# Kernel optimization log

Hardware: AMD Instinct MI355X
Metric: run time of the kernel (lower is better)

The kernel has to match this reference:

```python
import jax, jax.numpy as jnp
import numpy as np

EMBED_DIM = 1024
NUM_HEADS = 16
HEAD_DIM = EMBED_DIM // NUM_HEADS
SCALING = HEAD_DIM ** (-0.5)
LN_EPS = 1e-5


def setup_inputs() -> dict:
    key = jax.random.key(0)
    ks = jax.random.split(key, 6)
    N, L, D = 2, 2048, EMBED_DIM
    x = jax.random.normal(ks[0], (N, L, D), dtype=jnp.float32)
    W_in = jax.random.normal(ks[1], (3 * D, D), dtype=jnp.float32) * 0.02
    b_in = jnp.zeros((3 * D,), dtype=jnp.float32)
    Wc = jax.random.normal(ks[2], (HEAD_DIM, HEAD_DIM), dtype=jnp.float32) * 0.1
    bc = jnp.zeros((HEAD_DIM,), dtype=jnp.float32)
    ln_gamma = jnp.ones((HEAD_DIM,), dtype=jnp.float32)
    ln_beta = jnp.zeros((HEAD_DIM,), dtype=jnp.float32)
    W_out = jax.random.normal(ks[3], (D, D), dtype=jnp.float32) * 0.02
    b_out = jnp.zeros((D,), dtype=jnp.float32)
    return {"x": x, "W_in": W_in, "b_in": b_in, "Wc": Wc, "bc": bc,
            "ln_gamma": ln_gamma, "ln_beta": ln_beta, "W_out": W_out, "b_out": b_out}


def _reshape_heads(t, N, L):
    # (N, L, D) -> (N*H, L, head_dim)
    return t.reshape(N, L, NUM_HEADS, HEAD_DIM).transpose(0, 2, 1, 3).reshape(N * NUM_HEADS, L, HEAD_DIM)


def reference(x, W_in, b_in, Wc, bc, ln_gamma, ln_beta, W_out, b_out):
    N, L, D = x.shape
    qkv = jnp.einsum('nld,ed->nle', x, W_in) + b_in  # (N, L, 3D)
    q, k, v = jnp.split(qkv, 3, axis=-1)
    q_head = _reshape_heads(q, N, L)  # (B, L, HD) with B = N*H
    k_head = _reshape_heads(k, N, L)
    v_head = _reshape_heads(v, N, L)

    # Conv1d with kernel_size=1 == pointwise linear on head_dim channels
    q_temp = jnp.einsum('blc,oc->blo', q_head, Wc) + bc
    q_temp = jax.nn.gelu(q_temp, approximate=False)  # torch nn.GELU() is exact erf
    mu = q_temp.mean(axis=-1, keepdims=True)
    var = q_temp.var(axis=-1, keepdims=True)
    q_temp = (q_temp - mu) / jnp.sqrt(var + LN_EPS) * ln_gamma + ln_beta

    q_rel = q_temp.mean(axis=1)  # (B, HD) -- mean over sequence
    # one kernel row per (batch, head): (B, L)
    W_kernel_row = jnp.einsum('bd,bld->bl', q_rel * SCALING, k_head)

    # Toeplitz attention matrix: attn[b, i, j] = W_kernel_row[b, |i-j|]
    idx = jnp.arange(L)
    lags = jnp.abs(idx[:, None] - idx[None, :])  # (L, L), already in [0, L-1]
    attn = W_kernel_row[:, lags]  # (B, L, L) gather

    causal_mask = lags * jnp.sign(idx[None, :] - idx[:, None]) > 0  # j > i
    causal_mask = jnp.triu(jnp.ones((L, L), dtype=bool), k=1)
    attn = jnp.where(causal_mask[None, :, :], -jnp.inf, attn)
    weights = jax.nn.softmax(attn, axis=-1)  # (B, L, L); dropout=0 -> identity

    attn_out = jnp.einsum('bij,bjd->bid', weights, v_head)  # (B, L, HD)
    attn_out = attn_out.reshape(N, NUM_HEADS, L, HEAD_DIM).transpose(0, 2, 1, 3).reshape(N, L, D)
    output = jnp.einsum('nld,ed->nle', attn_out, W_out) + b_out
    return output, weights.mean(axis=1)
```

## Files before the change

kernel.cpp:

```cpp
#include <hip/hip_runtime.h>
#include <math.h>

#define L_SEQ 2048
#define D_EMB 1024
#define NHEADS 16
#define HD 64
#define BHEADS 32
#define NBATCH 2
#define LN_EPS 1e-5f
#define SCALING 0.125f

typedef __attribute__((ext_vector_type(8))) __bf16 bf16x8;
typedef __attribute__((ext_vector_type(4))) float f32x4;
typedef const __attribute__((address_space(1))) unsigned int* gptr_as1;
typedef __attribute__((address_space(3))) unsigned int* lptr_as3;

__device__ __forceinline__ void load16_to_lds(const void* g, void* l) {
  __builtin_amdgcn_global_load_lds((gptr_as1)g, (lptr_as3)l, 16, 0, 0);
}

__device__ __forceinline__ unsigned short f2bf(float f) {
  unsigned int u = __float_as_uint(f);
  u += 0x7fff + ((u >> 16) & 1);
  return (unsigned short)(u >> 16);
}

__global__ __launch_bounds__(256) void cvt4_bf16_kernel(
    const float* __restrict__ a, int na, const float* __restrict__ b, int nb,
    const float* __restrict__ c, int nc, const float* __restrict__ d, int nd,
    unsigned short* __restrict__ oa, unsigned short* __restrict__ ob,
    unsigned short* __restrict__ oc, unsigned short* __restrict__ od) {
  int i = (blockIdx.x * 256 + threadIdx.x) * 4;
  const float* src;
  unsigned short* dst;
  int j;
  if (i < na) { src = a; dst = oa; j = i; }
  else if (i < na + nb) { src = b; dst = ob; j = i - na; }
  else if (i < na + nb + nc) { src = c; dst = oc; j = i - na - nb; }
  else if (i < na + nb + nc + nd) { src = d; dst = od; j = i - na - nb - nc; }
  else return;
  float4 v = *(const float4*)&src[j];
  ushort4 o;
  o.x = f2bf(v.x); o.y = f2bf(v.y); o.z = f2bf(v.z); o.w = f2bf(v.w);
  *(ushort4*)&dst[j] = o;
}

__global__ __launch_bounds__(256) void gemm_qkv(
    const unsigned short* __restrict__ A, const unsigned short* __restrict__ B,
    const float* __restrict__ bias, unsigned short* __restrict__ Cbf,
    unsigned short* __restrict__ vT, int M, int Nn, int K) {
  __shared__ unsigned short As[4096];
  __shared__ unsigned short Bs[4096];
  const int id = blockIdx.y * 24 + blockIdx.x;
  const int by = (id / 48) * 2 + (id & 1);
  const int bx = (id % 48) >> 1;
  const int bm = by * 128;
  const int bn = bx * 128;
  const int tid = threadIdx.x;
  const int lane = tid & 63;
  const int wave = tid >> 6;
  const int wr = (wave >> 1) * 64;
  const int wc = (wave & 1) * 64;

  const int c0 = tid, c1 = tid + 256;
  const unsigned short* ga0 = A + (size_t)(bm + (c0 >> 6) * 16 + (c0 & 15)) * K + ((c0 >> 4) & 3) * 8;
  const unsigned short* ga1 = A + (size_t)(bm + (c1 >> 6) * 16 + (c1 & 15)) * K + ((c1 >> 4) & 3) * 8;
  const unsigned short* gb0 = B + (size_t)(bn + (c0 >> 6) * 16 + (c0 & 15)) * K + ((c0 >> 4) & 3) * 8;
  const unsigned short* gb1 = B + (size_t)(bn + (c1 >> 6) * 16 + (c1 & 15)) * K + ((c1 >> 4) & 3) * 8;

  f32x4 acc[4][4] = {};
  for (int k0 = 0; k0 < K; k0 += 32) {
    load16_to_lds(ga0 + k0, &As[c0 * 8]);
    load16_to_lds(ga1 + k0, &As[c1 * 8]);
    load16_to_lds(gb0 + k0, &Bs[c0 * 8]);
    load16_to_lds(gb1 + k0, &Bs[c1 * 8]);
    __syncthreads();
    bf16x8 af[4], bf[4];
    #pragma unroll
    for (int i = 0; i < 4; ++i)
      af[i] = *(const bf16x8*)&As[((wr >> 4) + i) * 512 + lane * 8];
    #pragma unroll
    for (int j = 0; j < 4; ++j)
      bf[j] = *(const bf16x8*)&Bs[((wc >> 4) + j) * 512 + lane * 8];
    #pragma unroll
    for (int i = 0; i < 4; ++i)
      #pragma unroll
      for (int j = 0; j < 4; ++j)
        acc[i][j] = __builtin_amdgcn_mfma_f32_16x16x32_bf16(af[i], bf[j], acc[i][j], 0, 0, 0);
    __syncthreads();
  }
  const int lc = lane & 15;
  const int lr4 = (lane >> 4) << 2;
  float bv[4];
  #pragma unroll
  for (int j = 0; j < 4; ++j) bv[j] = bias[bn + wc + j * 16 + lc];
  if (bn < 2 * D_EMB) {
    #pragma unroll
    for (int i = 0; i < 4; ++i)
      #pragma unroll
      for (int r = 0; r < 4; ++r) {
        const int row = bm + wr + i * 16 + lr4 + r;
        unsigned short* cp = &Cbf[(size_t)row * Nn + bn + wc + lc];
        #pragma unroll
        for (int j = 0; j < 4; ++j) cp[j * 16] = f2bf(acc[i][j][r] + bv[j]);
      }
  } else {
    #pragma unroll
    for (int i = 0; i < 4; ++i) {
      const int row0 = bm + wr + i * 16 + lr4;
      const int n = row0 >> 11;
      const int jseq = row0 & (L_SEQ - 1);
      #pragma unroll
      for (int j = 0; j < 4; ++j) {
        const int col = bn + wc + j * 16 + lc;
        const int d = col & 63;
        const int h = (col >> 6) & 15;
        ushort4 o;
        o.x = f2bf(acc[i][j][0] + bv[j]);
        o.y = f2bf(acc[i][j][1] + bv[j]);
        o.z = f2bf(acc[i][j][2] + bv[j]);
        o.w = f2bf(acc[i][j][3] + bv[j]);
        *(ushort4*)&vT[(size_t)((n * 16 + h) * 64 + d) * L_SEQ + jseq] = o;
      }
    }
  }
}

__global__ __launch_bounds__(256) void gemm_out64(
    const unsigned short* __restrict__ A, const unsigned short* __restrict__ B,
    const float* __restrict__ bias, float* __restrict__ C,
    int M, int Nn, int K) {
  __shared__ unsigned short As[2048];
  __shared__ unsigned short Bs[4096];
  const int bm = blockIdx.y * 64;
  const int bn = blockIdx.x * 128;
  const int tid = threadIdx.x;
  const int lane = tid & 63;
  const int wave = tid >> 6;
  const int wr = (wave >> 1) * 32;
  const int wc = (wave & 1) * 64;

  const int ca = tid;
  const int cb0 = tid, cb1 = tid + 256;
  const unsigned short* ga = A + (size_t)(bm + (ca >> 6) * 16 + (ca & 15)) * K + ((ca >> 4) & 3) * 8;
  const unsigned short* gb0 = B + (size_t)(bn + (cb0 >> 6) * 16 + (cb0 & 15)) * K + ((cb0 >> 4) & 3) * 8;
  const unsigned short* gb1 = B + (size_t)(bn + (cb1 >> 6) * 16 + (cb1 & 15)) * K + ((cb1 >> 4) & 3) * 8;

  f32x4 acc[2][4] = {};
  for (int k0 = 0; k0 < K; k0 += 32) {
    load16_to_lds(ga + k0, &As[ca * 8]);
    load16_to_lds(gb0 + k0, &Bs[cb0 * 8]);
    load16_to_lds(gb1 + k0, &Bs[cb1 * 8]);
    __syncthreads();
    bf16x8 af[2], bf[4];
    #pragma unroll
    for (int i = 0; i < 2; ++i)
      af[i] = *(const bf16x8*)&As[((wr >> 4) + i) * 512 + lane * 8];
    #pragma unroll
    for (int j = 0; j < 4; ++j)
      bf[j] = *(const bf16x8*)&Bs[((wc >> 4) + j) * 512 + lane * 8];
    #pragma unroll
    for (int i = 0; i < 2; ++i)
      #pragma unroll
      for (int j = 0; j < 4; ++j)
        acc[i][j] = __builtin_amdgcn_mfma_f32_16x16x32_bf16(af[i], bf[j], acc[i][j], 0, 0, 0);
    __syncthreads();
  }
  const int lc = lane & 15;
  const int lr4 = (lane >> 4) << 2;
  float bv[4];
  #pragma unroll
  for (int j = 0; j < 4; ++j) bv[j] = bias[bn + wc + j * 16 + lc];
  #pragma unroll
  for (int i = 0; i < 2; ++i)
    #pragma unroll
    for (int r = 0; r < 4; ++r) {
      const int row = bm + wr + i * 16 + lr4 + r;
      float* cp = &C[(size_t)row * Nn + bn + wc + lc];
      #pragma unroll
      for (int j = 0; j < 4; ++j) cp[j * 16] = acc[i][j][r] + bv[j];
    }
}

__global__ __launch_bounds__(256) void qtemp_mfma_kernel(
    const unsigned short* __restrict__ qkv_bf, const unsigned short* __restrict__ Wc_bf,
    const float* __restrict__ bc, const float* __restrict__ gamma,
    const float* __restrict__ beta, float* __restrict__ q_rel_sum) {
  __shared__ unsigned short Qs[8192];
  __shared__ unsigned short Ws[4096];
  __shared__ float red[4][64];
  const int b = blockIdx.y;
  const int n = b >> 4, h = b & 15;
  const int l0 = blockIdx.x * 128;
  const int tid = threadIdx.x;
  const int lane = tid & 63;
  const int wave = tid >> 6;
  const int quad = lane >> 4;
  const int mi = lane & 15;

  #pragma unroll
  for (int s = 0; s < 4; ++s) {
    const int c = tid + s * 256;
    const int row = ((c >> 7) << 4) + (c & 15);
    const int kof = ((c >> 4) & 7) << 3;
    load16_to_lds(qkv_bf + (size_t)(n * L_SEQ + l0 + row) * (3 * D_EMB) + h * 64 + kof,
                  &Qs[c * 8]);
  }
  #pragma unroll
  for (int s = 0; s < 2; ++s) {
    const int c = tid + s * 256;
    const int row = ((c >> 7) << 4) + (c & 15);
    const int kof = ((c >> 4) & 7) << 3;
    load16_to_lds(Wc_bf + row * 64 + kof, &Ws[c * 8]);
  }
  __syncthreads();

  f32x4 acc[2][4] = {};
  #pragma unroll
  for (int kk = 0; kk < 2; ++kk) {
    const int fo = ((kk * 4 + quad) * 16 + mi) * 8;
    bf16x8 bf[4];
    #pragma unroll
    for (int t = 0; t < 4; ++t) bf[t] = *(const bf16x8*)&Ws[t * 1024 + fo];
    #pragma unroll
    for (int isub = 0; isub < 2; ++isub) {
      const bf16x8 af = *(const bf16x8*)&Qs[(wave * 2 + isub) * 1024 + fo];
      #pragma unroll
      for (int t = 0; t < 4; ++t)
        acc[isub][t] = __builtin_amdgcn_mfma_f32_16x16x32_bf16(af, bf[t], acc[isub][t], 0, 0, 0);
    }
  }

  float bcv[4], gav[4], bev[4], colacc[4];
  #pragma unroll
  for (int t = 0; t < 4; ++t) {
    const int col = t * 16 + mi;
    bcv[t] = bc[col]; gav[t] = gamma[col]; bev[t] = beta[col];
    colacc[t] = 0.f;
  }
  #pragma unroll
  for (int isub = 0; isub < 2; ++isub) {
    #pragma unroll
    for (int r = 0; r < 4; ++r) {
      float g[4];
      float s1 = 0.f, s2 = 0.f;
      #pragma unroll
      for (int t = 0; t < 4; ++t) {
        const float d = acc[isub][t][r] + bcv[t];
        const float gg = 0.5f * d * (1.f + erff(d * 0.70710678118654752f));
        g[t] = gg;
        s1 += gg;
        s2 += gg * gg;
      }
      #pragma unroll
      for (int off = 8; off > 0; off >>= 1) {
        s1 += __shfl_xor(s1, off);
        s2 += __shfl_xor(s2, off);
      }
      const float mu = s1 * (1.f / 64.f);
      const float var = s2 * (1.f / 64.f) - mu * mu;
      const float rs = rsqrtf(var + LN_EPS);
      #pragma unroll
      for (int t = 0; t < 4; ++t)
        colacc[t] += (g[t] - mu) * rs * gav[t] + bev[t];
    }
  }
  #pragma unroll
  for (int t = 0; t < 4; ++t) {
    colacc[t] += __shfl_xor(colacc[t], 16);
    colacc[t] += __shfl_xor(colacc[t], 32);
  }
  if (quad == 0) {
    #pragma unroll
    for (int t = 0; t < 4; ++t) red[wave][t * 16 + mi] = colacc[t];
  }
  __syncthreads();
  if (wave == 0) {
    float tot = red[0][lane] + red[1][lane] + red[2][lane] + red[3][lane];
    atomicAdd(&q_rel_sum[b * 64 + lane], tot);
  }
}

__global__ __launch_bounds__(256) void wrow_kernel(
    const unsigned short* __restrict__ qkv_bf, const float* __restrict__ q_rel_sum,
    float* __restrict__ w_row) {
  const int b = blockIdx.x;
  const int n = b >> 4, h = b & 15;
  __shared__ float q_s[64];
  const int tid = threadIdx.x;
  if (tid < 64) q_s[tid] = q_rel_sum[b * 64 + tid] * (SCALING / (float)L_SEQ);
  __syncthreads();
  const int t = blockIdx.y * 256 + tid;
  const unsigned short* kp = &qkv_bf[(size_t)(n * L_SEQ + t) * (3 * D_EMB) + D_EMB + h * 64];
  float acc = 0.f;
  #pragma unroll
  for (int c = 0; c < 64; c += 8) {
    uint4 kv = *(const uint4*)&kp[c];
    acc += q_s[c + 0] * __uint_as_float(kv.x << 16);
    acc += q_s[c + 1] * __uint_as_float(kv.x & 0xffff0000u);
    acc += q_s[c + 2] * __uint_as_float(kv.y << 16);
    acc += q_s[c + 3] * __uint_as_float(kv.y & 0xffff0000u);
    acc += q_s[c + 4] * __uint_as_float(kv.z << 16);
    acc += q_s[c + 5] * __uint_as_float(kv.z & 0xffff0000u);
    acc += q_s[c + 6] * __uint_as_float(kv.w << 16);
    acc += q_s[c + 7] * __uint_as_float(kv.w & 0xffff0000u);
  }
  w_row[b * L_SEQ + t] = acc;
}

__global__ __launch_bounds__(256) void scan_kernel(
    const float* __restrict__ w_row, float* __restrict__ e_out,
    float* __restrict__ inv_out) {
  const int b = blockIdx.x;
  const int tid = threadIdx.x;
  __shared__ float sh[L_SEQ];
  __shared__ float ts[256];
  const float* wb = w_row + b * L_SEQ;
  float m = -3.4e38f;
  for (int i = tid; i < L_SEQ; i += 256) {
    float v = wb[i];
    sh[i] = v;
    m = fmaxf(m, v);
  }
  ts[tid] = m;
  __syncthreads();
  for (int off = 128; off > 0; off >>= 1) {
    if (tid < off) ts[tid] = fmaxf(ts[tid], ts[tid + off]);
    __syncthreads();
  }
  const float mx = ts[0];
  __syncthreads();
  const int t0 = tid * 8;
  float loc[8];
  float run = 0.f;
  #pragma unroll
  for (int k = 0; k < 8; ++k) {
    float ev = expf(sh[t0 + k] - mx);
    e_out[b * L_SEQ + t0 + k] = ev;
    run += ev;
    loc[k] = run;
  }
  ts[tid] = run;
  __syncthreads();
  for (int off = 1; off < 256; off <<= 1) {
    float v = ts[tid];
    float add = (tid >= off) ? ts[tid - off] : 0.f;
    __syncthreads();
    ts[tid] = v + add;
    __syncthreads();
  }
  float prefix = (tid > 0) ? ts[tid - 1] : 0.f;
  #pragma unroll
  for (int k = 0; k < 8; ++k)
    inv_out[b * L_SEQ + t0 + k] = 1.f / (prefix + loc[k]);
}

__global__ __launch_bounds__(256) void conv_mfma_kernel(
    const unsigned short* __restrict__ vT, const float* __restrict__ e_arr,
    const float* __restrict__ inv_arr, unsigned short* __restrict__ attn_out) {
  __shared__ unsigned short V_s[2][2048];
  __shared__ unsigned short rep[2][8 * 320];
  const int blk = 7 - blockIdx.x;
  const int b = blockIdx.y;
  const int dh = blockIdx.z;
  const int n = b >> 4, h = b & 15;
  const int blkI = blk * 256;
  const int blk4 = blk * 4;
  const int njt = blk4 + 4;
  const int tid = threadIdx.x;
  const int lane = tid & 63;
  const int wave = tid >> 6;
  const int quad = lane >> 4;
  const int mi = lane & 15;
  const float* e_b = e_arr + b * L_SEQ;

  const unsigned short* vsrc = vT +
      (size_t)(b * 64 + dh * 32 + (tid >> 7) * 16 + (tid & 15)) * L_SEQ + ((tid >> 4) & 7) * 8;

  f32x4 acc[4][2] = {};

  {
    load16_to_lds(vsrc, &V_s[0][tid * 8]);
    const int lagBase = blkI;
    int v = tid;
    int lag = lagBase + 256 - v;
    float ev = (lag >= 0 && lag < L_SEQ) ? e_b[lag] : 0.f;
    unsigned short bfv = f2bf(ev);
    #pragma unroll
    for (int r = 0; r < 8; ++r) { int idx = v - r; if (idx >= 0) rep[0][r * 320 + idx] = bfv; }
    if (tid < 64) {
      v = tid + 256;
      lag = lagBase - tid;
      ev = (lag >= 0 && lag < L_SEQ) ? e_b[lag] : 0.f;
      bfv = f2bf(ev);
      #pragma unroll
      for (int r = 0; r < 8; ++r) rep[0][r * 320 + (v - r)] = bfv;
    }
  }

  for (int jt = 0; jt < njt; ++jt) {
    __syncthreads();
    const int cb = jt & 1;
    if (jt + 1 < njt) {
      const int pb = cb ^ 1;
      const int j0 = (jt + 1) * 64;
      load16_to_lds(vsrc + j0, &V_s[pb][tid * 8]);
      const int lagBase = blkI - j0;
      int v = tid;
      int lag = lagBase + 256 - v;
      float ev = (lag >= 0 && lag < L_SEQ) ? e_b[lag] : 0.f;
      unsigned short bfv = f2bf(ev);
      #pragma unroll
      for (int r = 0; r < 8; ++r) { int idx = v - r; if (idx >= 0) rep[pb][r * 320 + idx] = bfv; }
      if (tid < 64) {
        v = tid + 256;
        lag = lagBase - tid;
        ev = (lag >= 0 && lag < L_SEQ) ? e_b[lag] : 0.f;
        bfv = f2bf(ev);
        #pragma unroll
        for (int r = 0; r < 8; ++r) rep[pb][r * 320 + (v - r)] = bfv;
      }
    }
    if (jt <= blk4 + wave) {
      const unsigned short* Vb = V_s[cb];
      const unsigned short* Rb = rep[cb];
      bf16x8 ef[6];
      #pragma unroll
      for (int q = 0; q < 6; ++q) {
        const int s = 256 - wave * 64 - mi + quad * 8 - 16 * (q - 2);
        const int rr = s & 7;
        ef[q] = *(const bf16x8*)&Rb[rr * 320 + (s - rr)];
      }
      #pragma unroll
      for (int kk = 0; kk < 2; ++kk) {
        bf16x8 bv[2];
        #pragma unroll
        for (int t = 0; t < 2; ++t)
          bv[t] = *(const bf16x8*)&Vb[t * 1024 + kk * 512 + lane * 8];
        #pragma unroll
        for (int isub = 0; isub < 4; ++isub) {
          const int qi = isub - 2 * kk + 2;
          #pragma unroll
          for (int t = 0; t < 2; ++t)
            acc[isub][t] = __builtin_amdgcn_mfma_f32_16x16x32_bf16(ef[qi], bv[t], acc[isub][t], 0, 0, 0);
        }
      }
    }
  }
  #pragma unroll
  for (int isub = 0; isub < 4; ++isub) {
    #pragma unroll
    for (int r = 0; r < 4; ++r) {
      const int i = blkI + wave * 64 + isub * 16 + quad * 4 + r;
      const float iv = inv_arr[b * L_SEQ + i];
      unsigned short* op = &attn_out[((size_t)(n * L_SEQ + i)) * D_EMB + h * 64 + dh * 32 + mi];
      #pragma unroll
      for (int t = 0; t < 2; ++t) op[t * 16] = f2bf(acc[isub][t][r] * iv);
    }
  }
}

__global__ __launch_bounds__(256) void wmean_kernel(
    const float* __restrict__ e_arr, const float* __restrict__ inv_arr,
    float* __restrict__ out_wm) {
  const int b = blockIdx.x;
  __shared__ float e_s[L_SEQ];
  __shared__ float inv_s[L_SEQ];
  __shared__ float red[256];
  const int tid = threadIdx.x;
  for (int i = tid; i < L_SEQ; i += 256) {
    e_s[i] = e_arr[b * L_SEQ + i];
    inv_s[i] = inv_arr[b * L_SEQ + i];
  }
  __syncthreads();
  const int jj = tid & 127;
  const int h2 = tid >> 7;
  const int j = blockIdx.y * 128 + jj;
  float acc = 0.f;
  for (int d = h2; j + d < L_SEQ; d += 2) acc += e_s[d] * inv_s[j + d];
  red[tid] = acc;
  __syncthreads();
  if (tid < 128)
    out_wm[b * L_SEQ + j] = (red[tid] + red[tid + 128]) * (1.f / (float)L_SEQ);
}

extern "C" void kernel_launch(void* const* d_in, const int* in_sizes, int n_in,
                              void* d_out, int out_size, void* d_ws, size_t ws_size,
                              hipStream_t stream) {
  const float* x       = (const float*)d_in[0];
  const float* W_in    = (const float*)d_in[1];
  const float* b_in    = (const float*)d_in[2];
  const float* Wc      = (const float*)d_in[3];
  const float* bc      = (const float*)d_in[4];
  const float* gamma   = (const float*)d_in[5];
  const float* beta    = (const float*)d_in[6];
  const float* W_out   = (const float*)d_in[7];
  const float* b_out   = (const float*)d_in[8];
  float* out = (float*)d_out;

  const int M = NBATCH * L_SEQ;
  char* ws = (char*)d_ws;
  unsigned short* xa_bf  = (unsigned short*)ws;
  unsigned short* Win_bf = (unsigned short*)(ws + 8388608);
  unsigned short* Wout_bf= (unsigned short*)(ws + 14680064);
  unsigned short* qkv_bf = (unsigned short*)(ws + 16777216);
  unsigned short* vT     = (unsigned short*)(ws + 41943040);
  float* q_rel = (float*)(ws + 50331648);
  float* e_arr = (float*)(ws + 50339840);
  float* inv_a = (float*)(ws + 50601984);
  float* w_row = (float*)(ws + 50864128);
  unsigned short* Wc_bf  = (unsigned short*)(ws + 51126272);

  hipMemsetAsync(q_rel, 0, BHEADS * HD * sizeof(float), stream);

  {
    const int na = M * D_EMB, nb = 3 * D_EMB * D_EMB, nc = D_EMB * D_EMB, nd = HD * HD;
    cvt4_bf16_kernel<<<dim3((na + nb + nc + nd) / 1024), 256, 0, stream>>>(
        x, na, W_in, nb, W_out, nc, Wc, nd, xa_bf, Win_bf, Wout_bf, Wc_bf);
  }
  gemm_qkv<<<dim3(24, 32), 256, 0, stream>>>(
      xa_bf, Win_bf, b_in, qkv_bf, vT, M, 3 * D_EMB, D_EMB);
  qtemp_mfma_kernel<<<dim3(16, BHEADS), 256, 0, stream>>>(
      qkv_bf, Wc_bf, bc, gamma, beta, q_rel);
  wrow_kernel<<<dim3(BHEADS, 8), 256, 0, stream>>>(qkv_bf, q_rel, w_row);
  scan_kernel<<<dim3(BHEADS), 256, 0, stream>>>(w_row, e_arr, inv_a);
  wmean_kernel<<<dim3(BHEADS, L_SEQ / 128), 256, 0, stream>>>(
      e_arr, inv_a, out + (size_t)M * D_EMB);
  conv_mfma_kernel<<<dim3(8, BHEADS, 2), 256, 0, stream>>>(vT, e_arr, inv_a, xa_bf);
  gemm_out64<<<dim3(D_EMB / 128, M / 64), 256, 0, stream>>>(
      xa_bf, Wout_bf, b_out, out, M, D_EMB, D_EMB);
}
```

Measured before the change: 277.4 us.

## Skip K projection by folding q_rel into W_k to compute kernel row from x

The input projection no longer computes K. The kernel row is now obtained as x·(W_kᵀ q_rel) plus q_rel·b_k, which removes one third of the QKV GEMM and the K writes to memory. The zw kernel builds z = W_kᵀ q_rel per head and then dots it with each bf16 x row over 1024 elements, so this step now reads the full x rather than 64-wide K slices. The q_rel atomics and the memset are replaced by per-block partial sums that are reduced deterministically. Each (head, chunk) block recomputes z redundantly, and rounding changes because K is no longer rounded to bf16.

Result: slower. 283.7 us (+2.3%).

```diff
diff --git a/kernel.cpp b/kernel.cpp
--- a/kernel.cpp
+++ b/kernel.cpp
@@ -23,6 +23,12 @@
   unsigned int u = __float_as_uint(f);
   u += 0x7fff + ((u >> 16) & 1);
   return (unsigned short)(u >> 16);
+}
+
+__device__ __forceinline__ float bflo(unsigned int u) { return __uint_as_float(u << 16); }
+__device__ __forceinline__ float bfhi(unsigned int u) { return __uint_as_float(u & 0xffff0000u); }
+__device__ __forceinline__ float bf2f(unsigned short us) {
+  return __uint_as_float((unsigned int)us << 16);
 }
 
 __global__ __launch_bounds__(256) void cvt4_bf16_kernel(
@@ -45,17 +51,18 @@
   *(ushort4*)&dst[j] = o;
 }
 
-__global__ __launch_bounds__(256) void gemm_qkv(
+__global__ __launch_bounds__(256) void gemm_qv(
     const unsigned short* __restrict__ A, const unsigned short* __restrict__ B,
-    const float* __restrict__ bias, unsigned short* __restrict__ Cbf,
-    unsigned short* __restrict__ vT, int M, int Nn, int K) {
+    const float* __restrict__ bias, unsigned short* __restrict__ qbf,
+    unsigned short* __restrict__ vT, int K) {
   __shared__ unsigned short As[4096];
   __shared__ unsigned short Bs[4096];
-  const int id = blockIdx.y * 24 + blockIdx.x;
-  const int by = (id / 48) * 2 + (id & 1);
-  const int bx = (id % 48) >> 1;
+  const int id = blockIdx.y * 16 + blockIdx.x;
+  const int by = (id >> 5) * 2 + (id & 1);
+  const int bx = (id & 31) >> 1;
   const int bm = by * 128;
   const int bn = bx * 128;
+  const int woff = (bn < D_EMB) ? 0 : D_EMB;
   const int tid = threadIdx.x;
   const int lane = tid & 63;
   const int wave = tid >> 6;
@@ -65,8 +72,8 @@
   const int c0 = tid, c1 = tid + 256;
   const unsigned short* ga0 = A + (size_t)(bm + (c0 >> 6) * 16 + (c0 & 15)) * K + ((c0 >> 4) & 3) * 8;
   const unsigned short* ga1 = A + (size_t)(bm + (c1 >> 6) * 16 + (c1 & 15)) * K + ((c1 >> 4) & 3) * 8;
-  const unsigned short* gb0 = B + (size_t)(bn + (c0 >> 6) * 16 + (c0 & 15)) * K + ((c0 >> 4) & 3) * 8;
-  const unsigned short* gb1 = B + (size_t)(bn + (c1 >> 6) * 16 + (c1 & 15)) * K + ((c1 >> 4) & 3) * 8;
+  const unsigned short* gb0 = B + (size_t)(bn + woff + (c0 >> 6) * 16 + (c0 & 15)) * K + ((c0 >> 4) & 3) * 8;
+  const unsigned short* gb1 = B + (size_t)(bn + woff + (c1 >> 6) * 16 + (c1 & 15)) * K + ((c1 >> 4) & 3) * 8;
 
   f32x4 acc[4][4] = {};
   for (int k0 = 0; k0 < K; k0 += 32) {
@@ -93,14 +100,14 @@
   const int lr4 = (lane >> 4) << 2;
   float bv[4];
   #pragma unroll
-  for (int j = 0; j < 4; ++j) bv[j] = bias[bn + wc + j * 16 + lc];
-  if (bn < 2 * D_EMB) {
+  for (int j = 0; j < 4; ++j) bv[j] = bias[bn + woff + wc + j * 16 + lc];
+  if (bn < D_EMB) {
     #pragma unroll
     for (int i = 0; i < 4; ++i)
       #pragma unroll
       for (int r = 0; r < 4; ++r) {
         const int row = bm + wr + i * 16 + lr4 + r;
-        unsigned short* cp = &Cbf[(size_t)row * Nn + bn + wc + lc];
+        unsigned short* cp = &qbf[(size_t)row * D_EMB + bn + wc + lc];
         #pragma unroll
         for (int j = 0; j < 4; ++j) cp[j * 16] = f2bf(acc[i][j][r] + bv[j]);
       }
@@ -112,9 +119,9 @@
       const int jseq = row0 & (L_SEQ - 1);
       #pragma unroll
       for (int j = 0; j < 4; ++j) {
-        const int col = bn + wc + j * 16 + lc;
-        const int d = col & 63;
-        const int h = (col >> 6) & 15;
+        const int cv = (bn - D_EMB) + wc + j * 16 + lc;
+        const int d = cv & 63;
+        const int h = cv >> 6;
         ushort4 o;
         o.x = f2bf(acc[i][j][0] + bv[j]);
         o.y = f2bf(acc[i][j][1] + bv[j]);
@@ -183,9 +190,9 @@
 }
 
 __global__ __launch_bounds__(256) void qtemp_mfma_kernel(
-    const unsigned short* __restrict__ qkv_bf, const unsigned short* __restrict__ Wc_bf,
+    const unsigned short* __restrict__ q_bf, const unsigned short* __restrict__ Wc_bf,
     const float* __restrict__ bc, const float* __restrict__ gamma,
-    const float* __restrict__ beta, float* __restrict__ q_rel_sum) {
+    const float* __restrict__ beta, float* __restrict__ q_rel_part) {
   __shared__ unsigned short Qs[8192];
   __shared__ unsigned short Ws[4096];
   __shared__ float red[4][64];
@@ -203,7 +210,7 @@
     const int c = tid + s * 256;
     const int row = ((c >> 7) << 4) + (c & 15);
     const int kof = ((c >> 4) & 7) << 3;
-    load16_to_lds(qkv_bf + (size_t)(n * L_SEQ + l0 + row) * (3 * D_EMB) + h * 64 + kof,
+    load16_to_lds(q_bf + (size_t)(n * L_SEQ + l0 + row) * D_EMB + h * 64 + kof,
                   &Qs[c * 8]);
   }
   #pragma unroll
@@ -277,33 +284,67 @@
   __syncthreads();
   if (wave == 0) {
     float tot = red[0][lane] + red[1][lane] + red[2][lane] + red[3][lane];
-    atomicAdd(&q_rel_sum[b * 64 + lane], tot);
-  }
-}
-
-__global__ __launch_bounds__(256) void wrow_kernel(
-    const unsigned short* __restrict__ qkv_bf, const float* __restrict__ q_rel_sum,
+    q_rel_part[((size_t)b * 16 + blockIdx.x) * 64 + lane] = tot;
+  }
+}
+
+__global__ __launch_bounds__(256) void zw_kernel(
+    const float* __restrict__ part, const unsigned short* __restrict__ Win_bf,
+    const float* __restrict__ b_in, const unsigned short* __restrict__ x_bf,
     float* __restrict__ w_row) {
   const int b = blockIdx.x;
   const int n = b >> 4, h = b & 15;
-  __shared__ float q_s[64];
-  const int tid = threadIdx.x;
-  if (tid < 64) q_s[tid] = q_rel_sum[b * 64 + tid] * (SCALING / (float)L_SEQ);
+  const int tid = threadIdx.x;
+  __shared__ float qrel[64];
+  __shared__ float zsh[1024];
+  __shared__ float ts[64];
+  __shared__ float kbs;
+  if (tid < 64) {
+    float s = 0.f;
+    #pragma unroll
+    for (int c = 0; c < 16; ++c) s += part[((size_t)b * 16 + c) * 64 + tid];
+    qrel[tid] = s;
+    ts[tid] = s * b_in[D_EMB + h * 64 + tid];
+  }
+  __syncthreads();
+  if (tid == 0) {
+    float kb = 0.f;
+    #pragma unroll
+    for (int d = 0; d < 64; ++d) kb += ts[d];
+    kbs = kb * (SCALING / (float)L_SEQ);
+  }
+  {
+    const int j0 = tid * 4;
+    float4 z4 = make_float4(0.f, 0.f, 0.f, 0.f);
+    const unsigned short* wp = Win_bf + (size_t)(D_EMB + h * 64) * D_EMB + j0;
+    #pragma unroll 4
+    for (int d = 0; d < 64; ++d) {
+      ushort4 w4 = *(const ushort4*)(wp + (size_t)d * D_EMB);
+      const float qd = qrel[d];
+      z4.x += qd * bf2f(w4.x);
+      z4.y += qd * bf2f(w4.y);
+      z4.z += qd * bf2f(w4.z);
+      z4.w += qd * bf2f(w4.w);
+    }
+    const float sc = SCALING / (float)L_SEQ;
+    zsh[j0 + 0] = z4.x * sc;
+    zsh[j0 + 1] = z4.y * sc;
+    zsh[j0 + 2] = z4.z * sc;
+    zsh[j0 + 3] = z4.w * sc;
+  }
   __syncthreads();
   const int t = blockIdx.y * 256 + tid;
-  const unsigned short* kp = &qkv_bf[(size_t)(n * L_SEQ + t) * (3 * D_EMB) + D_EMB + h * 64];
-  float acc = 0.f;
-  #pragma unroll
-  for (int c = 0; c < 64; c += 8) {
-    uint4 kv = *(const uint4*)&kp[c];
-    acc += q_s[c + 0] * __uint_as_float(kv.x << 16);
-    acc += q_s[c + 1] * __uint_as_float(kv.x & 0xffff0000u);
-    acc += q_s[c + 2] * __uint_as_float(kv.y << 16);
-    acc += q_s[c + 3] * __uint_as_float(kv.y & 0xffff0000u);
-    acc += q_s[c + 4] * __uint_as_float(kv.z << 16);
-    acc += q_s[c + 5] * __uint_as_float(kv.z & 0xffff0000u);
-    acc += q_s[c + 6] * __uint_as_float(kv.w << 16);
-    acc += q_s[c + 7] * __uint_as_float(kv.w & 0xffff0000u);
+  const unsigned short* xr = x_bf + (size_t)(n * L_SEQ + t) * D_EMB;
+  float acc = kbs;
+  #pragma unroll 4
+  for (int c = 0; c < D_EMB; c += 8) {
+    float4 zl = *(const float4*)&zsh[c];
+    float4 zh = *(const float4*)&zsh[c + 4];
+    uint4 xv = *(const uint4*)&xr[c];
+    acc += zl.x * bflo(xv.x) + zl.y * bfhi(xv.x)
+         + zl.z * bflo(xv.y) + zl.w * bfhi(xv.y)
+         + zh.x * bflo(xv.z) + zh.y * bfhi(xv.z)
+         + zh.z * bflo(xv.w) + zh.w * bfhi(xv.w);
   }
   w_row[b * L_SEQ + t] = acc;
 }
@@ -503,26 +544,23 @@
   unsigned short* xa_bf  = (unsigned short*)ws;
   unsigned short* Win_bf = (unsigned short*)(ws + 8388608);
   unsigned short* Wout_bf= (unsigned short*)(ws + 14680064);
-  unsigned short* qkv_bf = (unsigned short*)(ws + 16777216);
-  unsigned short* vT     = (unsigned short*)(ws + 41943040);
-  float* q_rel = (float*)(ws + 50331648);
-  float* e_arr = (float*)(ws + 50339840);
-  float* inv_a = (float*)(ws + 50601984);
-  float* w_row = (float*)(ws + 50864128);
-  unsigned short* Wc_bf  = (unsigned short*)(ws + 51126272);
-
-  hipMemsetAsync(q_rel, 0, BHEADS * HD * sizeof(float), stream);
+  unsigned short* Wc_bf  = (unsigned short*)(ws + 16777216);
+  unsigned short* q_bf   = (unsigned short*)(ws + 16785408);
+  unsigned short* vT     = (unsigned short*)(ws + 25174016);
+  float* part  = (float*)(ws + 33562624);
+  float* w_row = (float*)(ws + 33693696);
+  float* e_arr = (float*)(ws + 33955840);
+  float* inv_a = (float*)(ws + 34217984);
 
   {
     const int na = M * D_EMB, nb = 3 * D_EMB * D_EMB, nc = D_EMB * D_EMB, nd = HD * HD;
     cvt4_bf16_kernel<<<dim3((na + nb + nc + nd) / 1024), 256, 0, stream>>>(
         x, na, W_in, nb, W_out, nc, Wc, nd, xa_bf, Win_bf, Wout_bf, Wc_bf);
   }
-  gemm_qkv<<<dim3(24, 32), 256, 0, stream>>>(
-      xa_bf, Win_bf, b_in, qkv_bf, vT, M, 3 * D_EMB, D_EMB);
+  gemm_qv<<<dim3(16, 32), 256, 0, stream>>>(xa_bf, Win_bf, b_in, q_bf, vT, D_EMB);
   qtemp_mfma_kernel<<<dim3(16, BHEADS), 256, 0, stream>>>(
-      qkv_bf, Wc_bf, bc, gamma, beta, q_rel);
-  wrow_kernel<<<dim3(BHEADS, 8), 256, 0, stream>>>(qkv_bf, q_rel, w_row);
+      q_bf, Wc_bf, bc, gamma, beta, part);
+  zw_kernel<<<dim3(BHEADS, 8), 256, 0, stream>>>(part, Win_bf, b_in, xa_bf, w_row);
   scan_kernel<<<dim3(BHEADS), 256, 0, stream>>>(w_row, e_arr, inv_a);
   wmean_kernel<<<dim3(BHEADS, L_SEQ / 128), 256, 0, stream>>>(
       e_arr, inv_a, out + (size_t)M * D_EMB);
```
